# Kernel tuning notes

Measured on AMD Instinct MI355X. Metric: run time of the kernel, lower is better.

Reference implementation:

```python
import jax, jax.numpy as jnp
import numpy as np

N_HEAD = 16
D_MODEL = 1024


def setup_inputs() -> dict:
    key = jax.random.key(0)
    k1, k2, k3, k4, k5, k6 = jax.random.split(key, 6)
    B, S, D = 2, 2048, D_MODEL
    src = jax.random.normal(k1, (B, S, D), dtype=jnp.float32)
    attn_mask = jax.random.uniform(k2, (B, S, S), dtype=jnp.float32)
    # torch nn.Linear(d, 3d) / nn.Linear(d, d) params; stored as (in, out) for x @ W
    scale = 1.0 / np.sqrt(D)
    W_qkv = jax.random.uniform(k3, (D, 3 * D), dtype=jnp.float32, minval=-scale, maxval=scale)
    b_qkv = jax.random.uniform(k4, (3 * D,), dtype=jnp.float32, minval=-scale, maxval=scale)
    W_out = jax.random.uniform(k5, (D, D), dtype=jnp.float32, minval=-scale, maxval=scale)
    b_out = jax.random.uniform(k6, (D,), dtype=jnp.float32, minval=-scale, maxval=scale)
    return {"src": src, "attn_mask": attn_mask, "W_qkv": W_qkv, "b_qkv": b_qkv,
            "W_out": W_out, "b_out": b_out}


def reference(src, attn_mask, W_qkv, b_qkv, W_out, b_out):
    B, S, D = src.shape
    H = N_HEAD
    dh = D // H
    # broadcast mask [B,S,S] -> [B,1,S,S] (matches torch unsqueeze(1))
    mask = attn_mask[:, None, :, :]
    qkv = src @ W_qkv + b_qkv                      # [B,S,3D]
    q, k, v = jnp.split(qkv, 3, axis=-1)
    q = q.reshape(B, S, H, dh).transpose(0, 2, 1, 3)   # [B,H,S,dh]
    k = k.reshape(B, S, H, dh).transpose(0, 2, 1, 3)
    v = v.reshape(B, S, H, dh).transpose(0, 2, 1, 3)
    scores = jnp.einsum('bhqd,bhkd->bhqk', q, k) * (float(dh) ** -0.5)
    scores = scores * mask + (mask - 1.0) * 10000.0
    weights = jax.nn.softmax(scores, axis=-1)      # dropout_p=0 -> identity in eval/train
    out = jnp.einsum('bhqk,bhkd->bhqd', weights, v)
    out = out.transpose(0, 2, 1, 3).reshape(B, S, D)
    return out @ W_out + b_out
```

## Files before the change

### kernel.cpp

```cpp
#include <hip/hip_runtime.h>
#include <stdint.h>

#define SEQ    2048
#define DMODEL 1024

typedef __bf16 bf16x8 __attribute__((ext_vector_type(8)));
typedef float  f32x4  __attribute__((ext_vector_type(4)));

typedef __attribute__((address_space(1))) const void CGV;
typedef __attribute__((address_space(3))) void LDSV;

__device__ __forceinline__ void load_lds16(const void* g, void* l) {
    __builtin_amdgcn_global_load_lds((CGV*)g, (LDSV*)l, 16, 0, 0);
}

__device__ __forceinline__ float fast_exp2(float x) { return __builtin_exp2f(x); }

__global__ __launch_bounds__(256)
void transpose_f32_to_bf16(const float* __restrict__ in, __bf16* __restrict__ out,
                           int R, int C)
{
    __shared__ float tile[32][33];
    const int t  = threadIdx.x;
    const int tx = t & 31, ty = t >> 5;
    const int c0 = blockIdx.x * 32;
    const int r0 = blockIdx.y * 32;
#pragma unroll
    for (int i = 0; i < 4; ++i)
        tile[ty + i * 8][tx] = in[(size_t)(r0 + ty + i * 8) * C + c0 + tx];
    __syncthreads();
#pragma unroll
    for (int i = 0; i < 4; ++i)
        out[(size_t)(c0 + ty + i * 8) * R + r0 + tx] = (__bf16)tile[tx][ty + i * 8];
}

__global__ __launch_bounds__(256)
void convert_f32_to_bf16(const float* __restrict__ in, __bf16* __restrict__ out)
{
    const int i = (blockIdx.x * 256 + threadIdx.x) * 8;
    float4 a = *(const float4*)(in + i);
    float4 b = *(const float4*)(in + i + 4);
    __bf16 tmp[8] = { (__bf16)a.x, (__bf16)a.y, (__bf16)a.z, (__bf16)a.w,
                      (__bf16)b.x, (__bf16)b.y, (__bf16)b.z, (__bf16)b.w };
    *(uint4*)(out + i) = *(uint4*)tmp;
}

__global__ __launch_bounds__(256)
void transpose_v(const __bf16* __restrict__ in, __bf16* __restrict__ out)
{
    __shared__ __bf16 tile[32][34];
    const int t  = threadIdx.x;
    const int tx = t & 31, ty = t >> 5;
    const int s0 = blockIdx.x * 32;
    const int d0 = blockIdx.y * 32;
    const int bh = blockIdx.z;
    const __bf16* ip = in  + (size_t)bh * SEQ * 64;
    __bf16*       op = out + (size_t)bh * 64 * SEQ;
#pragma unroll
    for (int i = 0; i < 4; ++i)
        tile[ty + i * 8][tx] = ip[(size_t)(s0 + ty + i * 8) * 64 + d0 + tx];
    __syncthreads();
#pragma unroll
    for (int i = 0; i < 4; ++i)
        op[(size_t)(d0 + ty + i * 8) * SEQ + s0 + tx] = tile[tx][ty + i * 8];
}

template<bool A_IS_F32>
__global__ __launch_bounds__(256)
void gemm_kernel(const void* __restrict__ Av, const __bf16* __restrict__ Bt,
                 const float* __restrict__ bias,
                 __bf16* __restrict__ Cq, __bf16* __restrict__ Ck,
                 __bf16* __restrict__ Cv, float* __restrict__ Cplain,
                 int K, int N, int mode)
{
    __shared__ __attribute__((aligned(16))) __bf16 As[128][32];
    __shared__ __attribute__((aligned(16))) __bf16 Bs[128][32];

    const int t    = threadIdx.x;
    const int wave = __builtin_amdgcn_readfirstlane(t >> 6);
    const int lane = t & 63;
    const int l15  = lane & 15;
    const int quad = lane >> 4;
    const int wm   = (wave >> 1) * 64;
    const int wn   = (wave & 1) * 64;
    const int m0   = blockIdx.y * 128;
    const int n0   = blockIdx.x * 128;

    const int arow  = lane >> 2;
    const int akoff = (lane & 3) * 8;

    f32x4 acc[4][4] = {};

    for (int k0 = 0; k0 < K; k0 += 32) {
        __syncthreads();
        if (A_IS_F32) {
            const float* A = (const float*)Av;
            int row = t >> 1, kk = (t & 1) * 16;
            const float* srcp = A + (size_t)(m0 + row) * K + k0 + kk;
            float4 v0 = *(const float4*)(srcp);
            float4 v1 = *(const float4*)(srcp + 4);
            float4 v2 = *(const float4*)(srcp + 8);
            float4 v3 = *(const float4*)(srcp + 12);
            __bf16 tmp[16] = {
                (__bf16)v0.x, (__bf16)v0.y, (__bf16)v0.z, (__bf16)v0.w,
                (__bf16)v1.x, (__bf16)v1.y, (__bf16)v1.z, (__bf16)v1.w,
                (__bf16)v2.x, (__bf16)v2.y, (__bf16)v2.z, (__bf16)v2.w,
                (__bf16)v3.x, (__bf16)v3.y, (__bf16)v3.z, (__bf16)v3.w };
            *(uint4*)(&As[row][kk])     = *(uint4*)(tmp);
            *(uint4*)(&As[row][kk + 8]) = *(uint4*)(tmp + 8);
        } else {
            const __bf16* A = (const __bf16*)Av;
#pragma unroll
            for (int p = 0; p < 2; ++p) {
                int slab = (wave * 2 + p) * 16;
                const __bf16* g = A + (size_t)(m0 + slab + arow) * K + k0 + akoff;
                load_lds16(g, &As[slab][0]);
            }
        }
#pragma unroll
        for (int p = 0; p < 2; ++p) {
            int slab = (wave * 2 + p) * 16;
            const __bf16* g = Bt + (size_t)(n0 + slab + arow) * K + k0 + akoff;
            load_lds16(g, &Bs[slab][0]);
        }
        __syncthreads();

        bf16x8 af[4], bfr[4];
#pragma unroll
        for (int mi = 0; mi < 4; ++mi)
            af[mi] = *(const bf16x8*)(&As[wm + mi * 16 + l15][quad * 8]);
#pragma unroll
        for (int ni = 0; ni < 4; ++ni)
            bfr[ni] = *(const bf16x8*)(&Bs[wn + ni * 16 + l15][quad * 8]);
#pragma unroll
        for (int mi = 0; mi < 4; ++mi)
#pragma unroll
            for (int ni = 0; ni < 4; ++ni)
                acc[mi][ni] = __builtin_amdgcn_mfma_f32_16x16x32_bf16(
                    af[mi], bfr[ni], acc[mi][ni], 0, 0, 0);
    }

#pragma unroll
    for (int mi = 0; mi < 4; ++mi) {
        int rowb = m0 + wm + mi * 16 + quad * 4;
#pragma unroll
        for (int ni = 0; ni < 4; ++ni) {
            int col = n0 + wn + ni * 16 + l15;
            float bia = bias[col];
#pragma unroll
            for (int r = 0; r < 4; ++r) {
                float v = acc[mi][ni][r] + bia;
                int rr = rowb + r;
                if (mode == 0) {
                    int b = rr >> 11;
                    int s = rr & 2047;
                    int part = col >> 10;
                    int rem  = col & 1023;
                    int h = rem >> 6;
                    int d = rem & 63;
                    __bf16* dst = (part == 0) ? Cq : (part == 1) ? Ck : Cv;
                    dst[(((size_t)(b * 16 + h)) * SEQ + s) * 64 + d] = (__bf16)v;
                } else {
                    Cplain[(size_t)rr * N + col] = v;
                }
            }
        }
    }
}

__global__ __launch_bounds__(256, 2)
void attn_kernel(const __bf16* __restrict__ Q, const __bf16* __restrict__ Kb,
                 const __bf16* __restrict__ Vtg, const float* __restrict__ mask,
                 __bf16* __restrict__ Out)
{
    __shared__ __attribute__((aligned(16))) __bf16 Kt[2][64 * 64];
    __shared__ __attribute__((aligned(16))) __bf16 Vt[2][64 * 64];
    __shared__ __attribute__((aligned(16))) __bf16 Ps[4][32 * 64];

    const int t    = threadIdx.x;
    const int wave = __builtin_amdgcn_readfirstlane(t >> 6);
    const int lane = t & 63;
    const int l15  = lane & 15;
    const int quad = lane >> 4;
    const int swq  = lane & 7;
    const int bh   = blockIdx.x;
    const int b    = bh >> 4;
    const int h    = bh & 15;
    const int q0   = blockIdx.y * 128 + wave * 32;

    const float C1 = 0.180336880f;
    const float C2 = 14426.9502f;

    const __bf16* Qp  = Q   + (size_t)bh * SEQ * 64;
    const __bf16* Kp  = Kb  + (size_t)bh * SEQ * 64;
    const __bf16* Vtp = Vtg + (size_t)bh * 64 * SEQ;
    const float*  Mrow0 = mask + (size_t)b * SEQ * SEQ + (size_t)(q0 + l15) * SEQ + quad * 4;
    const float*  Mrow1 = Mrow0 + (size_t)16 * SEQ;

    const int ch  = wave * 2;
    const int rw0 = ch * 8 + (lane >> 3);
    const int swz = ((lane & 7) ^ (lane >> 3)) * 8;
    const __bf16* kS0 = Kp  + (size_t)rw0 * 64 + swz;
    const __bf16* kS1 = Kp  + (size_t)(rw0 + 8) * 64 + swz;
    const __bf16* vS0 = Vtp + (size_t)rw0 * SEQ + swz;
    const __bf16* vS1 = Vtp + (size_t)(rw0 + 8) * SEQ + swz;

    bf16x8 qf00, qf01, qf10, qf11;
    qf00 = *(const bf16x8*)(Qp + (size_t)(q0 + l15) * 64 + quad * 8);
    qf01 = *(const bf16x8*)(Qp + (size_t)(q0 + l15) * 64 + 32 + quad * 8);
    qf10 = *(const bf16x8*)(Qp + (size_t)(q0 + 16 + l15) * 64 + quad * 8);
    qf11 = *(const bf16x8*)(Qp + (size_t)(q0 + 16 + l15) * 64 + 32 + quad * 8);

    f32x4 oacc0[4] = {}, oacc1[4] = {};
    float mrun0 = -1e30f, lrun0 = 0.f;
    float mrun1 = -1e30f, lrun1 = 0.f;

    load_lds16(kS0, &Kt[0][ch * 512]);
    load_lds16(kS1, &Kt[0][(ch + 1) * 512]);
    load_lds16(vS0, &Vt[0][ch * 512]);
    load_lds16(vS1, &Vt[0][(ch + 1) * 512]);
    f32x4 mk0[4], mk1[4];
#pragma unroll
    for (int nb = 0; nb < 4; ++nb) {
        mk0[nb] = *(const f32x4*)(Mrow0 + nb * 16);
        mk1[nb] = *(const f32x4*)(Mrow1 + nb * 16);
    }

    const char* PsW0 = (const char*)&Ps[wave][0] + l15 * 128;
    const char* PsW1 = PsW0 + 16 * 128;

#pragma unroll 2
    for (int tt = 0; tt < SEQ / 64; ++tt) {
        const int key0 = tt * 64;
        const int keyn = (key0 + 64 <= SEQ - 64) ? key0 + 64 : SEQ - 64;
        const int cur  = tt & 1;
        const char* kcur = (const char*)&Kt[cur][0];
        const char* vcur = (const char*)&Vt[cur][0];
        __bf16* knxt = &Kt[cur ^ 1][0];
        __bf16* vnxt = &Vt[cur ^ 1][0];

        asm volatile("s_waitcnt vmcnt(0)" ::: "memory");
        __builtin_amdgcn_s_barrier();
        __builtin_amdgcn_sched_barrier(0);

        load_lds16(kS0 + (size_t)keyn * 64, knxt + ch * 512);
        load_lds16(kS1 + (size_t)keyn * 64, knxt + (ch + 1) * 512);
        load_lds16(vS0 + keyn, vnxt + ch * 512);
        load_lds16(vS1 + keyn, vnxt + (ch + 1) * 512);
        __builtin_amdgcn_sched_barrier(0);

        f32x4 sa0[4], sa1[4];
#pragma unroll
        for (int nb = 0; nb < 4; ++nb) {
            const char* kb = kcur + (nb * 16 + l15) * 128;
            bf16x8 kf0 = *(const bf16x8*)(kb + (((quad) ^ swq) << 4));
            bf16x8 kf1 = *(const bf16x8*)(kb + (((4 + quad) ^ swq) << 4));
            f32x4 z0 = {}, z1 = {};
            z0 = __builtin_amdgcn_mfma_f32_16x16x32_bf16(kf0, qf00, z0, 0, 0, 0);
            z1 = __builtin_amdgcn_mfma_f32_16x16x32_bf16(kf0, qf10, z1, 0, 0, 0);
            z0 = __builtin_amdgcn_mfma_f32_16x16x32_bf16(kf1, qf01, z0, 0, 0, 0);
            z1 = __builtin_amdgcn_mfma_f32_16x16x32_bf16(kf1, qf11, z1, 0, 0, 0);
            sa0[nb] = z0;
            sa1[nb] = z1;
        }

#pragma unroll
        for (int nb = 0; nb < 4; ++nb)
#pragma unroll
            for (int r = 0; r < 4; ++r) {
                float t0 = __fmaf_rn(C1, sa0[nb][r], C2);
                float t1 = __fmaf_rn(C1, sa1[nb][r], C2);
                sa0[nb][r] = __fmaf_rn(mk0[nb][r], t0, -C2);
                sa1[nb][r] = __fmaf_rn(mk1[nb][r], t1, -C2);
            }
#pragma unroll
        for (int nb = 0; nb < 4; ++nb) {
            mk0[nb] = *(const f32x4*)(Mrow0 + keyn + nb * 16);
            mk1[nb] = *(const f32x4*)(Mrow1 + keyn + nb * 16);
        }

        float v0 = fmaxf(fmaxf(sa0[0][0], sa0[0][1]), fmaxf(sa0[0][2], sa0[0][3]));
        float v1 = fmaxf(fmaxf(sa1[0][0], sa1[0][1]), fmaxf(sa1[0][2], sa1[0][3]));
#pragma unroll
        for (int nb = 1; nb < 4; ++nb) {
            v0 = fmaxf(v0, fmaxf(fmaxf(sa0[nb][0], sa0[nb][1]), fmaxf(sa0[nb][2], sa0[nb][3])));
            v1 = fmaxf(v1, fmaxf(fmaxf(sa1[nb][0], sa1[nb][1]), fmaxf(sa1[nb][2], sa1[nb][3])));
        }
        v0 = fmaxf(v0, __shfl_xor(v0, 16));
        v1 = fmaxf(v1, __shfl_xor(v1, 16));
        v0 = fmaxf(v0, __shfl_xor(v0, 32));
        v1 = fmaxf(v1, __shfl_xor(v1, 32));

        float al0 = 1.f, al1 = 1.f;
        bool need = (v0 > mrun0 + 8.f) || (v1 > mrun1 + 8.f);
        if (__any(need)) {
            float nm0 = fmaxf(mrun0, v0);
            float nm1 = fmaxf(mrun1, v1);
            al0 = fast_exp2(mrun0 - nm0);
            al1 = fast_exp2(mrun1 - nm1);
            mrun0 = nm0;
            mrun1 = nm1;
            float a0[4], a1[4];
#pragma unroll
            for (int r = 0; r < 4; ++r) {
                a0[r] = __shfl(al0, quad * 4 + r);
                a1[r] = __shfl(al1, quad * 4 + r);
            }
#pragma unroll
            for (int cb = 0; cb < 4; ++cb)
#pragma unroll
                for (int r = 0; r < 4; ++r) {
                    oacc0[cb][r] *= a0[r];
                    oacc1[cb][r] *= a1[r];
                }
        }

        float ac0 = 0.f, ac1 = 0.f;
#pragma unroll
        for (int nb = 0; nb < 4; ++nb)
#pragma unroll
            for (int r = 0; r < 4; ++r) {
                float p0 = fast_exp2(sa0[nb][r] - mrun0);
                float p1 = fast_exp2(sa1[nb][r] - mrun1);
                sa0[nb][r] = p0;
                sa1[nb][r] = p1;
                ac0 += p0;
                ac1 += p1;
            }
        ac0 += __shfl_xor(ac0, 16);
        ac1 += __shfl_xor(ac1, 16);
        ac0 += __shfl_xor(ac0, 32);
        ac1 += __shfl_xor(ac1, 32);
        lrun0 = lrun0 * al0 + ac0;
        lrun1 = lrun1 * al1 + ac1;

#pragma unroll
        for (int nb = 0; nb < 4; ++nb) {
            union { __bf16 hh[4]; uint2 u; } p0, p1;
            p0.hh[0] = (__bf16)sa0[nb][0];
            p0.hh[1] = (__bf16)sa0[nb][1];
            p0.hh[2] = (__bf16)sa0[nb][2];
            p0.hh[3] = (__bf16)sa0[nb][3];
            p1.hh[0] = (__bf16)sa1[nb][0];
            p1.hh[1] = (__bf16)sa1[nb][1];
            p1.hh[2] = (__bf16)sa1[nb][2];
            p1.hh[3] = (__bf16)sa1[nb][3];
            const int so = (((nb * 2 + (quad >> 1)) ^ swq) << 4) + (quad & 1) * 8;
            *(uint2*)(PsW0 + so) = p0.u;
            *(uint2*)(PsW1 + so) = p1.u;
        }
        asm volatile("s_waitcnt lgkmcnt(0)" ::: "memory");
        __builtin_amdgcn_sched_barrier(0);

        bf16x8 pf00 = *(const bf16x8*)(PsW0 + (((quad) ^ swq) << 4));
        bf16x8 pf01 = *(const bf16x8*)(PsW0 + (((4 + quad) ^ swq) << 4));
        bf16x8 pf10 = *(const bf16x8*)(PsW1 + (((quad) ^ swq) << 4));
        bf16x8 pf11 = *(const bf16x8*)(PsW1 + (((4 + quad) ^ swq) << 4));

        __builtin_amdgcn_s_setprio(1);
#pragma unroll
        for (int cb = 0; cb < 4; ++cb) {
            const char* vb = vcur + (cb * 16 + l15) * 128;
            bf16x8 vf0 = *(const bf16x8*)(vb + (((quad) ^ swq) << 4));
            bf16x8 vf1 = *(const bf16x8*)(vb + (((4 + quad) ^ swq) << 4));
            oacc0[cb] = __builtin_amdgcn_mfma_f32_16x16x32_bf16(pf00, vf0, oacc0[cb], 0, 0, 0);
            oacc1[cb] = __builtin_amdgcn_mfma_f32_16x16x32_bf16(pf10, vf0, oacc1[cb], 0, 0, 0);
            oacc0[cb] = __builtin_amdgcn_mfma_f32_16x16x32_bf16(pf01, vf1, oacc0[cb], 0, 0, 0);
            oacc1[cb] = __builtin_amdgcn_mfma_f32_16x16x32_bf16(pf11, vf1, oacc1[cb], 0, 0, 0);
        }
        __builtin_amdgcn_s_setprio(0);
    }

    float l40[4], l41[4];
#pragma unroll
    for (int r = 0; r < 4; ++r) {
        l40[r] = __shfl(lrun0, quad * 4 + r);
        l41[r] = __shfl(lrun1, quad * 4 + r);
    }
#pragma unroll
    for (int cb = 0; cb < 4; ++cb) {
#pragma unroll
        for (int r = 0; r < 4; ++r) {
            int qq0 = q0 + quad * 4 + r;
            Out[((size_t)(b * SEQ + qq0)) * DMODEL + h * 64 + cb * 16 + l15] =
                (__bf16)(oacc0[cb][r] / l40[r]);
            Out[((size_t)(b * SEQ + qq0 + 16)) * DMODEL + h * 64 + cb * 16 + l15] =
                (__bf16)(oacc1[cb][r] / l41[r]);
        }
    }
}

extern "C" void kernel_launch(void* const* d_in, const int* in_sizes, int n_in,
                              void* d_out, int out_size, void* d_ws, size_t ws_size,
                              hipStream_t stream)
{
    const float* src  = nullptr;
    const float* mask = nullptr;
    const float* Wqkv = nullptr;
    const float* bqkv = nullptr;
    const float* Wout = nullptr;
    const float* bout = nullptr;
    for (int i = 0; i < n_in; ++i) {
        switch (in_sizes[i]) {
            case 4194304: src  = (const float*)d_in[i]; break;
            case 8388608: mask = (const float*)d_in[i]; break;
            case 3145728: Wqkv = (const float*)d_in[i]; break;
            case 3072:    bqkv = (const float*)d_in[i]; break;
            case 1048576: Wout = (const float*)d_in[i]; break;
            case 1024:    bout = (const float*)d_in[i]; break;
        }
    }
    float* out = (float*)d_out;

    const size_t NE = (size_t)2 * 16 * SEQ * 64;
    __bf16* Qb     = (__bf16*)d_ws;
    __bf16* Kb     = Qb + NE;
    __bf16* Vb     = Kb + NE;
    __bf16* Vtg    = Vb + NE;
    __bf16* Wqkv_t = Vtg + NE;
    __bf16* Wout_t = Wqkv_t + (size_t)3072 * 1024;
    __bf16* Ao     = Vb;
    __bf16* SrcBf  = Vtg;

    transpose_f32_to_bf16<<<dim3(3072 / 32, 1024 / 32), 256, 0, stream>>>(
        Wqkv, Wqkv_t, 1024, 3072);
    transpose_f32_to_bf16<<<dim3(1024 / 32, 1024 / 32), 256, 0, stream>>>(
        Wout, Wout_t, 1024, 1024);

    convert_f32_to_bf16<<<dim3(4194304 / (256 * 8)), 256, 0, stream>>>(src, SrcBf);

    gemm_kernel<false><<<dim3(3072 / 128, 4096 / 128), 256, 0, stream>>>(
        (const void*)SrcBf, Wqkv_t, bqkv, Qb, Kb, Vb, nullptr, 1024, 3072, 0);

    transpose_v<<<dim3(SEQ / 32, 2, 32), 256, 0, stream>>>(Vb, Vtg);

    attn_kernel<<<dim3(32, SEQ / 128), 256, 0, stream>>>(Qb, Kb, Vtg, mask, Ao);

    gemm_kernel<false><<<dim3(1024 / 128, 4096 / 128), 256, 0, stream>>>(
        (const void*)Ao, Wout_t, bout, nullptr, nullptr, nullptr, out, 1024, 1024, 1);
}
```

Before: 270.4 us.

## Double-buffer GEMM LDS tiles and halve attention block size

The GEMM now keeps two LDS buffers, so the async global-to-LDS loads for the next K-slice are issued before computing on the current one, and it needs one barrier per step instead of two. The unused f32 template path is removed. The attention kernel moves to 2-wave blocks covering 64 queries each. Every wave now stages 4 K/V rows per tile, the P scratch shrinks, and the grid doubles. The attention wait becomes vmcnt(8), which relies on outstanding-load ordering being right, and smaller blocks re-read K/V more often per query.

After: 265.1 us. About the same (-1.9%).

```diff
diff --git a/kernel.cpp b/kernel.cpp
--- a/kernel.cpp
+++ b/kernel.cpp
@@ -65,16 +65,15 @@
         op[(size_t)(d0 + ty + i * 8) * SEQ + s0 + tx] = tile[tx][ty + i * 8];
 }
 
-template<bool A_IS_F32>
 __global__ __launch_bounds__(256)
-void gemm_kernel(const void* __restrict__ Av, const __bf16* __restrict__ Bt,
+void gemm_kernel(const __bf16* __restrict__ A, const __bf16* __restrict__ Bt,
                  const float* __restrict__ bias,
                  __bf16* __restrict__ Cq, __bf16* __restrict__ Ck,
                  __bf16* __restrict__ Cv, float* __restrict__ Cplain,
                  int K, int N, int mode)
 {
-    __shared__ __attribute__((aligned(16))) __bf16 As[128][32];
-    __shared__ __attribute__((aligned(16))) __bf16 Bs[128][32];
+    __shared__ __attribute__((aligned(16))) __bf16 As[2][128][32];
+    __shared__ __attribute__((aligned(16))) __bf16 Bs[2][128][32];
 
     const int t    = threadIdx.x;
     const int wave = __builtin_amdgcn_readfirstlane(t >> 6);
@@ -91,54 +90,44 @@
 
     f32x4 acc[4][4] = {};
 
+#define GSTAGE(buf, kk)                                                        \
+    {                                                                          \
+        _Pragma("unroll")                                                      \
+        for (int p = 0; p < 2; ++p) {                                          \
+            int slab = (wave * 2 + p) * 16;                                    \
+            load_lds16(A  + (size_t)(m0 + slab + arow) * K + (kk) + akoff,     \
+                       &As[buf][slab][0]);                                     \
+            load_lds16(Bt + (size_t)(n0 + slab + arow) * K + (kk) + akoff,     \
+                       &Bs[buf][slab][0]);                                     \
+        }                                                                      \
+    }
+
+    GSTAGE(0, 0);
+    int cur = 0;
+#pragma unroll 2
     for (int k0 = 0; k0 < K; k0 += 32) {
-        __syncthreads();
-        if (A_IS_F32) {
-            const float* A = (const float*)Av;
-            int row = t >> 1, kk = (t & 1) * 16;
-            const float* srcp = A + (size_t)(m0 + row) * K + k0 + kk;
-            float4 v0 = *(const float4*)(srcp);
-            float4 v1 = *(const float4*)(srcp + 4);
-            float4 v2 = *(const float4*)(srcp + 8);
-            float4 v3 = *(const float4*)(srcp + 12);
-            __bf16 tmp[16] = {
-                (__bf16)v0.x, (__bf16)v0.y, (__bf16)v0.z, (__bf16)v0.w,
-                (__bf16)v1.x, (__bf16)v1.y, (__bf16)v1.z, (__bf16)v1.w,
-                (__bf16)v2.x, (__bf16)v2.y, (__bf16)v2.z, (__bf16)v2.w,
-                (__bf16)v3.x, (__bf16)v3.y, (__bf16)v3.z, (__bf16)v3.w };
-            *(uint4*)(&As[row][kk])     = *(uint4*)(tmp);
-            *(uint4*)(&As[row][kk + 8]) = *(uint4*)(tmp + 8);
-        } else {
-            const __bf16* A = (const __bf16*)Av;
-#pragma unroll
-            for (int p = 0; p < 2; ++p) {
-                int slab = (wave * 2 + p) * 16;
-                const __bf16* g = A + (size_t)(m0 + slab + arow) * K + k0 + akoff;
-                load_lds16(g, &As[slab][0]);
-            }
-        }
-#pragma unroll
-        for (int p = 0; p < 2; ++p) {
-            int slab = (wave * 2 + p) * 16;
-            const __bf16* g = Bt + (size_t)(n0 + slab + arow) * K + k0 + akoff;
-            load_lds16(g, &Bs[slab][0]);
-        }
-        __syncthreads();
+        asm volatile("s_waitcnt vmcnt(0)" ::: "memory");
+        __builtin_amdgcn_s_barrier();
+        __builtin_amdgcn_sched_barrier(0);
+        if (k0 + 32 < K) GSTAGE(cur ^ 1, k0 + 32);
+        __builtin_amdgcn_sched_barrier(0);
 
         bf16x8 af[4], bfr[4];
 #pragma unroll
         for (int mi = 0; mi < 4; ++mi)
-            af[mi] = *(const bf16x8*)(&As[wm + mi * 16 + l15][quad * 8]);
+            af[mi] = *(const bf16x8*)(&As[cur][wm + mi * 16 + l15][quad * 8]);
 #pragma unroll
         for (int ni = 0; ni < 4; ++ni)
-            bfr[ni] = *(const bf16x8*)(&Bs[wn + ni * 16 + l15][quad * 8]);
+            bfr[ni] = *(const bf16x8*)(&Bs[cur][wn + ni * 16 + l15][quad * 8]);
 #pragma unroll
         for (int mi = 0; mi < 4; ++mi)
 #pragma unroll
             for (int ni = 0; ni < 4; ++ni)
                 acc[mi][ni] = __builtin_amdgcn_mfma_f32_16x16x32_bf16(
                     af[mi], bfr[ni], acc[mi][ni], 0, 0, 0);
-    }
+        cur ^= 1;
+    }
+#undef GSTAGE
 
 #pragma unroll
     for (int mi = 0; mi < 4; ++mi) {
@@ -168,14 +157,14 @@
     }
 }
 
-__global__ __launch_bounds__(256, 2)
+__global__ __launch_bounds__(128, 2)
 void attn_kernel(const __bf16* __restrict__ Q, const __bf16* __restrict__ Kb,
                  const __bf16* __restrict__ Vtg, const float* __restrict__ mask,
                  __bf16* __restrict__ Out)
 {
     __shared__ __attribute__((aligned(16))) __bf16 Kt[2][64 * 64];
     __shared__ __attribute__((aligned(16))) __bf16 Vt[2][64 * 64];
-    __shared__ __attribute__((aligned(16))) __bf16 Ps[4][32 * 64];
+    __shared__ __attribute__((aligned(16))) __bf16 Ps[2][32 * 64];
 
     const int t    = threadIdx.x;
     const int wave = __builtin_amdgcn_readfirstlane(t >> 6);
@@ -186,7 +175,7 @@
     const int bh   = blockIdx.x;
     const int b    = bh >> 4;
     const int h    = bh & 15;
-    const int q0   = blockIdx.y * 128 + wave * 32;
+    const int q0   = blockIdx.y * 64 + wave * 32;
 
     const float C1 = 0.180336880f;
     const float C2 = 14426.9502f;
@@ -197,13 +186,15 @@
     const float*  Mrow0 = mask + (size_t)b * SEQ * SEQ + (size_t)(q0 + l15) * SEQ + quad * 4;
     const float*  Mrow1 = Mrow0 + (size_t)16 * SEQ;
 
-    const int ch  = wave * 2;
-    const int rw0 = ch * 8 + (lane >> 3);
     const int swz = ((lane & 7) ^ (lane >> 3)) * 8;
-    const __bf16* kS0 = Kp  + (size_t)rw0 * 64 + swz;
-    const __bf16* kS1 = Kp  + (size_t)(rw0 + 8) * 64 + swz;
-    const __bf16* vS0 = Vtp + (size_t)rw0 * SEQ + swz;
-    const __bf16* vS1 = Vtp + (size_t)(rw0 + 8) * SEQ + swz;
+    const __bf16* kS[4];
+    const __bf16* vS[4];
+#pragma unroll
+    for (int p = 0; p < 4; ++p) {
+        int rw = wave * 32 + p * 8 + (lane >> 3);
+        kS[p] = Kp  + (size_t)rw * 64 + swz;
+        vS[p] = Vtp + (size_t)rw * SEQ + swz;
+    }
 
     bf16x8 qf00, qf01, qf10, qf11;
     qf00 = *(const bf16x8*)(Qp + (size_t)(q0 + l15) * 64 + quad * 8);
@@ -215,10 +206,17 @@
     float mrun0 = -1e30f, lrun0 = 0.f;
     float mrun1 = -1e30f, lrun1 = 0.f;
 
-    load_lds16(kS0, &Kt[0][ch * 512]);
-    load_lds16(kS1, &Kt[0][(ch + 1) * 512]);
-    load_lds16(vS0, &Vt[0][ch * 512]);
-    load_lds16(vS1, &Vt[0][(ch + 1) * 512]);
+#define STAGE_KV(bufidx, key)                                                 \
+    {                                                                         \
+        _Pragma("unroll")                                                     \
+        for (int p = 0; p < 4; ++p) {                                         \
+            load_lds16(kS[p] + (size_t)(key) * 64,                            \
+                       &Kt[bufidx][(wave * 4 + p) * 512]);                    \
+            load_lds16(vS[p] + (key), &Vt[bufidx][(wave * 4 + p) * 512]);     \
+        }                                                                     \
+    }
+
+    STAGE_KV(0, 0);
     f32x4 mk0[4], mk1[4];
 #pragma unroll
     for (int nb = 0; nb < 4; ++nb) {
@@ -236,17 +234,12 @@
         const int cur  = tt & 1;
         const char* kcur = (const char*)&Kt[cur][0];
         const char* vcur = (const char*)&Vt[cur][0];
-        __bf16* knxt = &Kt[cur ^ 1][0];
-        __bf16* vnxt = &Vt[cur ^ 1][0];
-
-        asm volatile("s_waitcnt vmcnt(0)" ::: "memory");
+
+        asm volatile("s_waitcnt vmcnt(8)" ::: "memory");
         __builtin_amdgcn_s_barrier();
         __builtin_amdgcn_sched_barrier(0);
 
-        load_lds16(kS0 + (size_t)keyn * 64, knxt + ch * 512);
-        load_lds16(kS1 + (size_t)keyn * 64, knxt + (ch + 1) * 512);
-        load_lds16(vS0 + keyn, vnxt + ch * 512);
-        load_lds16(vS1 + keyn, vnxt + (ch + 1) * 512);
+        if (tt < SEQ / 64 - 1) STAGE_KV(cur ^ 1, key0 + 64);
         __builtin_amdgcn_sched_barrier(0);
 
         f32x4 sa0[4], sa1[4];
@@ -370,6 +363,7 @@
         }
         __builtin_amdgcn_s_setprio(0);
     }
+#undef STAGE_KV
 
     float l40[4], l41[4];
 #pragma unroll
@@ -429,13 +423,13 @@
 
     convert_f32_to_bf16<<<dim3(4194304 / (256 * 8)), 256, 0, stream>>>(src, SrcBf);
 
-    gemm_kernel<false><<<dim3(3072 / 128, 4096 / 128), 256, 0, stream>>>(
-        (const void*)SrcBf, Wqkv_t, bqkv, Qb, Kb, Vb, nullptr, 1024, 3072, 0);
+    gemm_kernel<<<dim3(3072 / 128, 4096 / 128), 256, 0, stream>>>(
+        SrcBf, Wqkv_t, bqkv, Qb, Kb, Vb, nullptr, 1024, 3072, 0);
 
     transpose_v<<<dim3(SEQ / 32, 2, 32), 256, 0, stream>>>(Vb, Vtg);
 
-    attn_kernel<<<dim3(32, SEQ / 128), 256, 0, stream>>>(Qb, Kb, Vtg, mask, Ao);
-
-    gemm_kernel<false><<<dim3(1024 / 128, 4096 / 128), 256, 0, stream>>>(
-        (const void*)Ao, Wout_t, bout, nullptr, nullptr, nullptr, out, 1024, 1024, 1);
-}
+    attn_kernel<<<dim3(32, SEQ / 64), 128, 0, stream>>>(Qb, Kb, Vtg, mask, Ao);
+
+    gemm_kernel<<<dim3(1024 / 128, 4096 / 128), 256, 0, stream>>>(
+        Ao, Wout_t, bout, nullptr, nullptr, nullptr, out, 1024, 1024, 1);
+}
```
